# Performance work log

Hardware: AMD Instinct MI355X
Metric: run time of the kernel (lower is better)

## Reference

```python
import itertools
import jax, jax.numpy as jnp
import numpy as np

# ---- config (mirrors args) ----
BS = 8; C = 20              # 4 + num_sem_categories
FH, FW = 480, 640           # frame height/width
DU = 2                      # du_scale
NSC = 16                    # num_sem_categories
RES = 5; ZRES = 5           # xy / z map resolution (cm)
MAP_CM = 4800 // 2          # map_size_cm // global_downscaling
VR = 100                    # vision_range
HFOV = 79.0
MAXH = int(200 / ZRES); MINH = int(-40 / ZRES)   # 40, -8
AGENT_H = 0.88 * 100.0
CAT_T, EXP_T, MAP_T = 5.0, 1.0, 1.0
STAIR_R = 30
DEG = 57.29577951308232
M = MAP_CM // RES           # 480 local map cells

CAM_XC = (FW - 1.) / 2.
CAM_ZC = (FH - 1.) / 2.
CAM_F = (FW / 2.) / np.tan(np.deg2rad(HFOV / 2.))
SHIFT_X = VR * RES // 2     # shift_loc theta = pi/2 -> identity rotation, +x only

def _circle_mask(r):
    size = 2 * r
    ii, jj = np.meshgrid(np.arange(size), np.arange(size), indexing='ij')
    return (((ii + 0.5 - size // 2) ** 2 + (jj + 0.5 - size // 2) ** 2) <= r ** 2).astype(np.float32)

CIRCLE = jnp.asarray(_circle_mask(STAIR_R))

def splat_feat_nd(init_grid, feat, coords):
    # init_grid [B,F,d0,d1,d2], feat [B,F,N], coords [B,3,N] in [-1,1]
    B, nF = init_grid.shape[:2]
    gd = init_grid.shape[2:]
    grid_flat = init_grid.reshape(B, nF, -1)
    pos_dim, wts_dim = [], []
    for d in range(3):
        pos = coords[:, d, :] * gd[d] / 2 + gd[d] / 2
        pd, wd = [], []
        for ix in (0, 1):
            pos_ix = jnp.floor(pos) + ix
            safe = ((pos_ix > 0) & (pos_ix < gd[d])).astype(pos.dtype)
            wd.append((1 - jnp.abs(pos - pos_ix)) * safe)
            pd.append(pos_ix * safe)
        pos_dim.append(pd); wts_dim.append(wd)
    idxs, vals = [], []
    for ix_d in itertools.product((0, 1), repeat=3):  # 8 trilinear corners
        index = jnp.zeros_like(pos_dim[0][0])
        wts = jnp.ones_like(wts_dim[0][0])
        for d in range(3):
            index = index * gd[d] + pos_dim[d][ix_d[d]]
            wts = wts * wts_dim[d][ix_d[d]]
        idxs.append(index.astype(jnp.int32))
        vals.append(feat * wts[:, None, :])
    idx = jnp.concatenate(idxs, -1)          # [B, 8N]
    val = jnp.concatenate(vals, -1)          # [B, F, 8N]
    grid_flat = jax.vmap(lambda g, i, v: g.at[:, i].add(v))(grid_flat, idx, val)
    return jnp.round(grid_flat).reshape(init_grid.shape)

def affine_grid(theta, H, W):
    # F.affine_grid, align_corners=False (torch default)
    xs = (jnp.arange(W, dtype=theta.dtype) + 0.5) * 2 / W - 1
    ys = (jnp.arange(H, dtype=theta.dtype) + 0.5) * 2 / H - 1
    gy, gx = jnp.meshgrid(ys, xs, indexing='ij')
    base = jnp.stack([gx, gy, jnp.ones_like(gx)], -1)   # [H,W,3]
    return jnp.einsum('bij,hwj->bhwi', theta, base)     # [B,H,W,2]

def grid_sample(img, grid):
    # bilinear, zero padding, align_corners=True
    B, C_, H, W = img.shape
    gx = (grid[..., 0] + 1.) * (W - 1) / 2.
    gy = (grid[..., 1] + 1.) * (H - 1) / 2.
    x0 = jnp.floor(gx); y0 = jnp.floor(gy)
    def gather(ix, iy):
        valid = ((ix >= 0) & (ix < W) & (iy >= 0) & (iy < H)).astype(img.dtype)
        ic = jnp.clip(ix, 0, W - 1).astype(jnp.int32)
        jc = jnp.clip(iy, 0, H - 1).astype(jnp.int32)
        v = jax.vmap(lambda im, yy, xx: im[:, yy, xx])(img, jc, ic)  # [B,C,H,W]
        return v * valid[:, None]
    wx1 = gx - x0; wx0 = 1 - wx1; wy1 = gy - y0; wy0 = 1 - wy1
    return (gather(x0, y0) * (wx0 * wy0)[:, None]
            + gather(x0 + 1, y0) * (wx1 * wy0)[:, None]
            + gather(x0, y0 + 1) * (wx0 * wy1)[:, None]
            + gather(x0 + 1, y0 + 1) * (wx1 * wy1)[:, None])

def maxpool3(x):
    return jax.lax.reduce_window(x, -jnp.inf, jax.lax.max,
                                 (1, 1, 3, 3), (1, 1, 1, 1),
                                 [(0, 0), (0, 0), (1, 1), (1, 1)])

def _forward(obs, pose_obs, maps_last, poses_last, eve_angle):
    bs, c, h, w = obs.shape
    hs, ws = h // DU, w // DU
    depth = obs[:, 3, ::DU, ::DU]
    # point cloud from depth (du.get_point_cloud_from_z_t)
    xg = jnp.arange(0, w, DU, dtype=obs.dtype)[None, None, :]
    zg = (h - 1 - jnp.arange(0, h, DU, dtype=obs.dtype))[None, :, None]
    X = (xg - CAM_XC) * depth / CAM_F
    Z = (zg - CAM_ZC) * depth / CAM_F
    # camera elevation rotation about x-axis (per-env eve_angle) + sensor height
    th = jnp.deg2rad(eve_angle)[:, None, None]
    ct, st = jnp.cos(th), jnp.sin(th)
    Yr = ct * depth - st * Z
    Zr = st * depth + ct * Z + AGENT_H
    Xs = X + SHIFT_X
    # normalize to [-1,1] voxel coords
    cx = (Xs / RES - VR // 2) / VR * 2.0
    cy = (Yr / RES - VR // 2) / VR * 2.0
    cz = (Zr / ZRES - (MAXH + MINH) // 2) / (MAXH - MINH) * 2.0
    coords = jnp.stack([cx.reshape(bs, -1), cy.reshape(bs, -1), cz.reshape(bs, -1)], 1)
    sem = obs[:, 4:].reshape(bs, c - 4, hs, DU, ws, DU).mean((3, 5))  # AvgPool2d(du)
    feat = jnp.concatenate([jnp.ones((bs, 1, hs * ws), obs.dtype),
                            sem.reshape(bs, c - 4, hs * ws)], 1)
    init_grid = jnp.zeros((bs, 1 + NSC, VR, VR, MAXH - MINH), obs.dtype)
    voxels = splat_feat_nd(init_grid, feat, coords).transpose(0, 1, 3, 2, 4)
    min_z = int(25 / ZRES - MINH)
    max_z = int((AGENT_H + 50) / ZRES - MINH)
    mid_z = int(AGENT_H / ZRES - MINH)
    ah_proj = voxels[..., min_z:max_z].sum(-1)
    stair_proj = voxels[..., mid_z - 5:mid_z].sum(-1)
    all_proj = voxels.sum(-1)
    fp_map = jnp.clip(ah_proj[:, 0:1] / MAP_T, 0., 1.)
    fp_stair = jnp.clip(stair_proj[:, 0:1] / MAP_T, 0., 1.)
    fp_exp = jnp.clip(all_proj[:, 0:1] / EXP_T, 0., 1.)
    x1 = M // 2 - VR // 2; x2 = x1 + VR; y1 = M // 2; y2 = y1 + VR
    agent_view = jnp.zeros((bs, c, M, M), obs.dtype)
    agent_view = agent_view.at[:, 0:1, y1:y2, x1:x2].set(fp_map)
    agent_view = agent_view.at[:, 1:2, y1:y2, x1:x2].set(fp_exp)
    agent_view = agent_view.at[:, 4:, y1:y2, x1:x2].set(jnp.clip(ah_proj[:, 1:] / CAT_T, 0., 1.))
    agent_view_stair = jax.lax.stop_gradient(agent_view).at[:, 0:1, y1:y2, x1:x2].set(fp_stair)
    # pose integration (get_new_pose_batch)
    tr = poses_last[:, 2] / DEG
    ny = poses_last[:, 1] + pose_obs[:, 0] * jnp.sin(tr) + pose_obs[:, 1] * jnp.cos(tr)
    nx = poses_last[:, 0] + pose_obs[:, 0] * jnp.cos(tr) - pose_obs[:, 1] * jnp.sin(tr)
    no = poses_last[:, 2] + pose_obs[:, 2] * DEG
    no = jnp.fmod(no - 180.0, 360.0) + 180.0
    no = jnp.fmod(no + 180.0, 360.0) - 180.0
    current_poses = jnp.stack([nx, ny, no], 1)
    cp = jax.lax.stop_gradient(current_poses)  # st_pose = clone().detach()
    half = M // 2
    st_xy = -(cp[:, :2] * 100.0 / RES - half) / half
    st_t = (90.0 - cp[:, 2]) * np.pi / 180.0
    c_, s_ = jnp.cos(st_t), jnp.sin(st_t)
    zeros = jnp.zeros_like(c_); ones = jnp.ones_like(c_)
    theta1 = jnp.stack([jnp.stack([c_, -s_, zeros], 1), jnp.stack([s_, c_, zeros], 1)], 1)
    theta2 = jnp.stack([jnp.stack([ones, zeros, st_xy[:, 0]], 1),
                        jnp.stack([zeros, ones, st_xy[:, 1]], 1)], 1)
    rot_grid = affine_grid(theta1, M, M)
    trans_grid = affine_grid(theta2, M, M)
    translated = grid_sample(grid_sample(agent_view, rot_grid), trans_grid)
    diff = translated[:, 1:2] - maxpool3(translated[:, 0:1])
    diff = jnp.where(diff > 0.8, 1.0, 0.0).astype(obs.dtype)
    maps2 = jnp.maximum(maps_last, translated)
    m0 = (eve_angle == 0)[:, None, None, None] & (diff == 1.0)
    map_pred = maps2.at[:, 0:1].set(jnp.where(m0, 0.0, maps2[:, 0:1]))
    # stair map
    translated_stair = grid_sample(grid_sample(agent_view_stair, rot_grid), trans_grid)
    s_y = jnp.clip((cp[0, 1] * 100 / 5).astype(jnp.int32), STAIR_R, M - STAIR_R - 1)
    s_x = jnp.clip((cp[0, 0] * 100 / 5).astype(jnp.int32), STAIR_R, M - STAIR_R - 1)
    full_mask = jax.lax.dynamic_update_slice(jnp.zeros((M, M), obs.dtype), CIRCLE.astype(obs.dtype),
                                             (s_y - STAIR_R, s_x - STAIR_R))
    translated_stair = translated_stair.at[0, 0:2].multiply(full_mask)
    diff_s = translated_stair[:, 1:2] - translated_stair[:, 0:1]
    diff_s = jnp.where(diff_s > 0.8, 1.0, 0.0).astype(obs.dtype)
    maps3 = jnp.maximum(maps_last, translated_stair)
    m0s = (eve_angle == 0)[:, None, None, None] & (diff_s == 1.0)
    map_pred_stair = maps3.at[:, 0:1].set(jnp.where(m0s, 0.0, maps3[:, 0:1]))
    return translated, map_pred, map_pred_stair, current_poses

def setup_inputs() -> dict:
    key = jax.random.key(0)
    k1, k2, k3, k4, k5 = jax.random.split(key, 5)
    obs = jax.random.uniform(k1, (BS, C, FH, FW), jnp.float32)
    depth = 50.0 + 350.0 * jax.random.uniform(k2, (BS, FH, FW), jnp.float32)  # depth in cm
    obs = obs.at[:, 3].set(depth)
    pose_obs = jax.random.normal(k3, (BS, 3), jnp.float32) * jnp.array([0.1, 0.05, 0.02], jnp.float32)
    maps_last = jax.random.uniform(k4, (BS, C, M, M), jnp.float32)
    poses_last = (jnp.tile(jnp.array([12.0, 12.0, 0.0], jnp.float32), (BS, 1))
                  + jax.random.normal(k5, (BS, 3), jnp.float32) * jnp.array([0.5, 0.5, 30.0], jnp.float32))
    eve_angle = jnp.array([0., 0., -30., 0., 30., 0., 0., 0.], jnp.float32)
    return {'obs': obs, 'pose_obs': pose_obs, 'maps_last': maps_last,
            'poses_last': poses_last, 'eve_angle': eve_angle}

def reference(obs, pose_obs, maps_last, poses_last, eve_angle):
    return _forward(obs, pose_obs, maps_last, poses_last, eve_angle)
```

## Files before the change

kernel.cpp:

```cpp
#include <hip/hip_runtime.h>
#include <cmath>

#define NBS 8
#define NC 20
#define NFH 480
#define NFW 640
#define NHS 240
#define NWS 320
#define NM 480
#define NPIX (NM * NM)
#define NVR 100
#define NPIXELS (NBS * NHS * NWS)
#define PPB (NHS * NWS)
#define CPB 4

constexpr long long T_OFF    = 0LL;
constexpr long long P_OFF    = 36864000LL;
constexpr long long S_OFF    = 73728000LL;
constexpr long long POSE_OFF = 110592000LL;

constexpr long long SMAP_OFF = P_OFF;
constexpr long long PAR_OFF  = SMAP_OFF + 1520000LL;
constexpr long long REC_OFF  = PAR_OFF + 64LL;
constexpr long long EPOS_OFF = REC_OFF + 2457600LL;
constexpr long long ESEM_OFF = EPOS_OFF + 2457600LL;
constexpr long long CNT_OFF  = ESEM_OFF + 9830400LL;
constexpr long long OFF2_OFF = CNT_OFF + 80000LL;
constexpr long long CUR_OFF  = OFF2_OFF + 80000LL;

__device__ __forceinline__ float clamp01(float x) {
    return fminf(fmaxf(x, 0.0f), 1.0f);
}

__device__ __forceinline__ void project_px(const float* __restrict__ ob, float ev,
                                           float camf, int iy, int ix,
                                           float& posx, float& posy, float& posz,
                                           bool& alive, bool& semz) {
    float depth = ob[(3LL * NFH + 2 * iy) * NFW + 2 * ix];
    float th = ev * 0.017453292519943295f;
    float ct = cosf(th), st = sinf(th);
    float X = ((float)(2 * ix) - 319.5f) * depth / camf;
    float Z = ((float)(479 - 2 * iy) - 239.5f) * depth / camf;
    float Yr = ct * depth - st * Z;
    float Zr = st * depth + ct * Z + 88.0f;
    float Xs = X + 250.0f;
    float cx = ((Xs / 5.0f) - 50.0f) / 100.0f * 2.0f;
    float cy = ((Yr / 5.0f) - 50.0f) / 100.0f * 2.0f;
    float cz = ((Zr / 5.0f) - 16.0f) / 48.0f * 2.0f;
    posx = (cx * 100.0f) / 2.0f + 50.0f;
    posy = (cy * 100.0f) / 2.0f + 50.0f;
    posz = (cz * 48.0f) / 2.0f + 24.0f;
    alive = (posx > 0.0f) && (posx < 100.0f) &&
            (posy > 0.0f) && (posy < 100.0f) &&
            (posz > 0.0f) && (posz < 48.0f);
    semz = (posz > 12.0f) && (posz < 35.0f);
}

__global__ void k_pose(const float* __restrict__ pose_obs,
                       const float* __restrict__ poses_last,
                       float* __restrict__ outp) {
    int b = threadIdx.x;
    if (b >= NBS) return;
    float* pose_out = outp + POSE_OFF;
    float* par = outp + PAR_OFF;
    const float DEGf = 57.29577951308232f;
    float tr = poses_last[b * 3 + 2] / DEGf;
    float s_tr = sinf(tr), c_tr = cosf(tr);
    float ny = poses_last[b * 3 + 1] + pose_obs[b * 3 + 0] * s_tr + pose_obs[b * 3 + 1] * c_tr;
    float nx = poses_last[b * 3 + 0] + pose_obs[b * 3 + 0] * c_tr - pose_obs[b * 3 + 1] * s_tr;
    float no = poses_last[b * 3 + 2] + pose_obs[b * 3 + 2] * DEGf;
    no = fmodf(no - 180.0f, 360.0f) + 180.0f;
    no = fmodf(no + 180.0f, 360.0f) - 180.0f;
    pose_out[b * 3 + 0] = nx;
    pose_out[b * 3 + 1] = ny;
    pose_out[b * 3 + 2] = no;
    float stx = -((nx * 100.0f) / 5.0f - 240.0f) / 240.0f;
    float sty = -((ny * 100.0f) / 5.0f - 240.0f) / 240.0f;
    float stt = ((90.0f - no) * 3.14159265358979323846f) / 180.0f;
    par[b * 4 + 0] = cosf(stt);
    par[b * 4 + 1] = sinf(stt);
    par[b * 4 + 2] = stx;
    par[b * 4 + 3] = sty;
    if (b == 0) {
        int sy = (int)((ny * 100.0f) / 5.0f);
        int sx = (int)((nx * 100.0f) / 5.0f);
        sy = min(max(sy, 30), NM - 31);
        sx = min(max(sx, 30), NM - 31);
        par[32] = (float)sy;
        par[33] = (float)sx;
    }
}

__global__ void k_count(const float* __restrict__ obs,
                        const float* __restrict__ eve, float camf,
                        unsigned int* __restrict__ counts,
                        float4* __restrict__ rec) {
    int tid = blockIdx.x * blockDim.x + threadIdx.x;
    if (tid >= NPIXELS) return;
    int b = tid / PPB;
    int p = tid % PPB;
    int iy = p / NWS, ix = p % NWS;
    const float* ob = obs + (long long)b * NC * NFH * NFW;
    float posx, posy, posz;
    bool alive, semz;
    project_px(ob, eve[b], camf, iy, ix, posx, posy, posz, alive, semz);
    float flag = alive ? (semz ? 2.0f : 1.0f) : 0.0f;
    rec[tid] = make_float4(posx, posy, posz, flag);
    if (!alive) return;
    int fx = (int)floorf(posx);
    int fy = (int)floorf(posy);
    atomicAdd(&counts[b * 10000 + fx * 100 + fy], 1u);
}

__global__ void __launch_bounds__(1024) k_scan(const unsigned int* __restrict__ counts,
                                               unsigned int* __restrict__ offs,
                                               unsigned int* __restrict__ curs) {
    int b = blockIdx.x;
    int t = threadIdx.x;
    int lane = t & 63, wid = t >> 6;
    const unsigned int* cb = counts + b * 10000;
    unsigned int base_i = (unsigned int)t * 10u;
    unsigned int v[10];
    unsigned int s = 0;
#pragma unroll
    for (int k = 0; k < 10; ++k) {
        unsigned int i = base_i + (unsigned int)k;
        unsigned int x = (i < 10000u) ? cb[i] : 0u;
        v[k] = s;
        s += x;
    }
    unsigned int incl = s;
#pragma unroll
    for (int d = 1; d < 64; d <<= 1) {
        unsigned int u = __shfl_up(incl, d);
        if (lane >= d) incl += u;
    }
    __shared__ unsigned int wtot[16];
    __shared__ unsigned int wexc[16];
    if (lane == 63) wtot[wid] = incl;
    __syncthreads();
    if (t == 0) {
        unsigned int a = 0;
        for (int i = 0; i < 16; ++i) { wexc[i] = a; a += wtot[i]; }
    }
    __syncthreads();
    unsigned int tbase = wexc[wid] + (incl - s);
#pragma unroll
    for (int k = 0; k < 10; ++k) {
        unsigned int i = base_i + (unsigned int)k;
        if (i < 10000u) {
            unsigned int e = tbase + v[k];
            offs[b * 10000 + i] = e;
            curs[b * 10000 + i] = e;
        }
    }
}

__global__ void k_fill(const float* __restrict__ obs,
                       const float4* __restrict__ rec,
                       unsigned int* __restrict__ curs,
                       float4* __restrict__ epos,
                       float4* __restrict__ esem4) {
    int tid = blockIdx.x * blockDim.x + threadIdx.x;
    if (tid >= NPIXELS) return;
    float4 r = rec[tid];
    if (r.w == 0.0f) return;
    int b = tid / PPB;
    int p = tid % PPB;
    int iy = p / NWS, ix = p % NWS;
    int fx = (int)floorf(r.x);
    int fy = (int)floorf(r.y);
    unsigned int slot = atomicAdd(&curs[b * 10000 + fx * 100 + fy], 1u);
    long long gslot = (long long)b * PPB + slot;
    epos[gslot] = make_float4(r.x, r.y, r.z, 0.0f);
    if (r.w == 2.0f) {
        const float* ob = obs + (long long)b * NC * NFH * NFW;
        float sem[16];
#pragma unroll
        for (int k = 0; k < 16; ++k) {
            const float* q = ob + ((long long)(4 + k) * NFH + 2 * iy) * NFW + 2 * ix;
            sem[k] = (q[0] + q[1] + q[NFW] + q[NFW + 1]) * 0.25f;
        }
#pragma unroll
        for (int g = 0; g < 4; ++g)
            esem4[gslot * 4 + g] =
                make_float4(sem[4 * g], sem[4 * g + 1], sem[4 * g + 2], sem[4 * g + 3]);
    }
}

__global__ void __launch_bounds__(256) k_accum(const float4* __restrict__ epos,
                                               const float4* __restrict__ esem4,
                                               const unsigned int* __restrict__ counts,
                                               const unsigned int* __restrict__ offs,
                                               float* __restrict__ smap) {
    int wid = threadIdx.x >> 6, lane = threadIdx.x & 63;
    int col = blockIdx.x * CPB + wid;
    int b = col / 10000;
    int xy = col % 10000;
    int x = xy / 100, y = xy % 100;
    __shared__ float acc[CPB][400];
    float* A = acc[wid];
    for (int i = lane; i < 400; i += 64) A[i] = 0.0f;
    __syncthreads();
    if (x >= 1 && y >= 1) {
        int base = b * 10000;
        int b00 = base + (x - 1) * 100 + (y - 1);
        int b01 = base + (x - 1) * 100 + y;
        int b10 = base + x * 100 + (y - 1);
        int b11 = base + x * 100 + y;
        unsigned int s0 = offs[b00];
        unsigned int n0 = offs[b01] + counts[b01] - s0;
        unsigned int s1 = offs[b10];
        unsigned int n1 = offs[b11] + counts[b11] - s1;
        unsigned int E = n0 + n1;
        const float4* pb = epos + (long long)b * PPB;
        const float4* sb = esem4 + (long long)b * PPB * 4;
        float fx_ = (float)x, fy_ = (float)y;
        for (unsigned int t = lane; t < E; t += 64) {
            unsigned int idx = (t < n0) ? (s0 + t) : (s1 + (t - n0));
            float4 e = pb[idx];
            float wx = 1.0f - fabsf(e.x - fx_);
            float wy = 1.0f - fabsf(e.y - fy_);
            float wxy = wx * wy;
            if (wxy <= 0.0f) continue;
            float posz = e.z;
            float fz = floorf(posz);
            bool zsem = (posz > 12.0f) && (posz < 35.0f);
            float sem[16];
            if (zsem) {
#pragma unroll
                for (int g = 0; g < 4; ++g) {
                    float4 s4 = sb[(long long)idx * 4 + g];
                    sem[4 * g + 0] = s4.x; sem[4 * g + 1] = s4.y;
                    sem[4 * g + 2] = s4.z; sem[4 * g + 3] = s4.w;
                }
            }
#pragma unroll
            for (int d = 0; d < 2; ++d) {
                float zf = fz + (float)d;
                int z = (int)zf;
                if (z < 1 || z > 47) continue;
                float w = wxy * (1.0f - fabsf(posz - zf));
                if (w == 0.0f) continue;
                atomicAdd(&A[z], w);
                if (z >= 13 && z < 35) {
                    float* ap = A + 48 + (z - 13) * 16;
#pragma unroll
                    for (int k = 0; k < 16; ++k)
                        atomicAdd(ap + k, sem[k] * w);
                }
            }
        }
    }
    __syncthreads();
    float* smb = smap + (long long)b * 19 * 10000;
    int ij = y * 100 + x;
    if (lane < 16) {
        float s = 0.0f;
#pragma unroll
        for (int z = 13; z < 35; ++z) s += rintf(A[48 + (z - 13) * 16 + lane]);
        smb[(3 + lane) * 10000 + ij] = clamp01(s / 5.0f);
    } else if (lane == 16) {
        float s = 0.0f;
        for (int z = 13; z < 35; ++z) s += rintf(A[z]);
        smb[ij] = clamp01(s);
    } else if (lane == 17) {
        float s = 0.0f;
        for (int z = 0; z < 48; ++z) s += rintf(A[z]);
        smb[10000 + ij] = clamp01(s);
    } else if (lane == 18) {
        float s = 0.0f;
        for (int z = 20; z < 25; ++z) s += rintf(A[z]);
        smb[20000 + ij] = clamp01(s);
    }
}

__global__ void k_translate(float* __restrict__ outp,
                            const float* __restrict__ smap,
                            const float* __restrict__ par,
                            const float* __restrict__ maps_last,
                            const float* __restrict__ eve) {
    int tid = blockIdx.x * blockDim.x + threadIdx.x;
    if (tid >= NBS * NPIX) return;
    int b = tid / NPIX;
    int ij = tid % NPIX;
    int i = ij / NM, j = ij % NM;
    float c = par[b * 4 + 0], s = par[b * 4 + 1];
    float stx = par[b * 4 + 2], sty = par[b * 4 + 3];
    float gx = (((float)j + 0.5f) * 2.0f) / 480.0f - 1.0f;
    float gy = (((float)i + 0.5f) * 2.0f) / 480.0f - 1.0f;
    float px = ((gx + stx) + 1.0f) * 479.0f / 2.0f;
    float py = ((gy + sty) + 1.0f) * 479.0f / 2.0f;
    float x0 = floorf(px), y0 = floorf(py);
    float wx1 = px - x0, wx0 = 1.0f - wx1;
    float wy1 = py - y0, wy0 = 1.0f - wy1;
    int offs[16];
    float wts[16];
    int nt = 0;
#pragma unroll
    for (int t = 0; t < 4; ++t) {
        int ox = t & 1, oy = t >> 1;
        float xo = x0 + (float)ox, yo = y0 + (float)oy;
        if (!(xo >= 0.0f && xo < 480.0f && yo >= 0.0f && yo < 480.0f)) continue;
        float wo = (ox ? wx1 : wx0) * (oy ? wy1 : wy0);
        int ixo = (int)xo, iyo = (int)yo;
        float gx2 = (((float)ixo + 0.5f) * 2.0f) / 480.0f - 1.0f;
        float gy2 = (((float)iyo + 0.5f) * 2.0f) / 480.0f - 1.0f;
        float rx = c * gx2 - s * gy2;
        float ry = s * gx2 + c * gy2;
        float qx = (rx + 1.0f) * 479.0f / 2.0f;
        float qy = (ry + 1.0f) * 479.0f / 2.0f;
        float xq0 = floorf(qx), yq0 = floorf(qy);
        float u1 = qx - xq0, u0 = 1.0f - u1;
        float v1 = qy - yq0, v0 = 1.0f - v1;
#pragma unroll
        for (int t2 = 0; t2 < 4; ++t2) {
            int ax = t2 & 1, ay = t2 >> 1;
            float xa = xq0 + (float)ax, ya = yq0 + (float)ay;
            if (xa >= 190.0f && xa < 290.0f && ya >= 240.0f && ya < 340.0f) {
                float w = wo * ((ax ? u1 : u0) * (ay ? v1 : v0));
                if (w != 0.0f) {
                    offs[nt] = ((int)ya - 240) * 100 + ((int)xa - 190);
                    wts[nt] = w;
                    ++nt;
                }
            }
        }
    }
    float a0 = 0.0f, a1 = 0.0f, as_ = 0.0f;
    float cat[16];
#pragma unroll
    for (int k = 0; k < 16; ++k) cat[k] = 0.0f;
    if (nt > 0) {
        const float* sm = smap + (long long)b * 19 * 10000;
        for (int t = 0; t < nt; ++t) {
            float w = wts[t];
            int o = offs[t];
            a0 += w * sm[o];
            a1 += w * sm[10000 + o];
            as_ += w * sm[20000 + o];
#pragma unroll
            for (int k = 0; k < 16; ++k) cat[k] += w * sm[(3 + k) * 10000 + o];
        }
    }
    float* To = outp + T_OFF;
    long long obase = (long long)b * NC * NPIX + ij;
    To[obase] = a0;
    To[obase + (long long)NPIX] = a1;
    To[obase + 2LL * NPIX] = 0.0f;
    To[obase + 3LL * NPIX] = 0.0f;
#pragma unroll
    for (int k = 0; k < 16; ++k) To[obase + (long long)(4 + k) * NPIX] = cat[k];
    float ts0 = as_, t1s = a1;
    if (b == 0) {
        float dy = (float)i - par[32] + 0.5f;
        float dx = (float)j - par[33] + 0.5f;
        float mask = (dy * dy + dx * dx <= 900.0f) ? 1.0f : 0.0f;
        ts0 *= mask;
        t1s *= mask;
    }
    bool eve0 = (eve[b] == 0.0f);
    bool flag = (t1s - ts0) > 0.8f;
    const float* ml = maps_last + (long long)b * NC * NPIX;
    float* So = outp + S_OFF;
#pragma unroll
    for (int ch = 0; ch < NC; ++ch) {
        float tch = (ch == 0) ? ts0 : (ch == 1) ? t1s
                  : (ch < 4) ? 0.0f : cat[ch - 4];
        float m3 = fmaxf(ml[(long long)ch * NPIX + ij], tch);
        So[obase + (long long)ch * NPIX] = (ch == 0 && eve0 && flag) ? 0.0f : m3;
    }
}

__global__ void k_pred(const float* __restrict__ T, const float* __restrict__ maps_last,
                       const float* __restrict__ eve, float* __restrict__ outP) {
    int tid = blockIdx.x * blockDim.x + threadIdx.x;
    if (tid >= NBS * NPIX) return;
    int b = tid / NPIX;
    int ij = tid % NPIX;
    int i = ij / NM, j = ij % NM;
    const float* Tb = T + (long long)b * NC * NPIX;
    float mp = -INFINITY;
#pragma unroll
    for (int di = -1; di <= 1; ++di) {
        int ii = i + di;
        if (ii < 0 || ii >= NM) continue;
#pragma unroll
        for (int dj = -1; dj <= 1; ++dj) {
            int jj = j + dj;
            if (jj < 0 || jj >= NM) continue;
            mp = fmaxf(mp, Tb[(long long)ii * NM + jj]);
        }
    }
    float t1 = Tb[(long long)NPIX + ij];
    bool flag = (t1 - mp) > 0.8f;
    bool eve0 = (eve[b] == 0.0f);
    const float* ml = maps_last + (long long)b * NC * NPIX;
    long long obase = (long long)b * NC * NPIX + ij;
#pragma unroll
    for (int ch = 0; ch < NC; ++ch) {
        float m2 = fmaxf(ml[(long long)ch * NPIX + ij], Tb[(long long)ch * NPIX + ij]);
        outP[obase + (long long)ch * NPIX] = (ch == 0 && eve0 && flag) ? 0.0f : m2;
    }
}

extern "C" void kernel_launch(void* const* d_in, const int* in_sizes, int n_in,
                              void* d_out, int out_size, void* d_ws, size_t ws_size,
                              hipStream_t stream) {
    const float* obs = (const float*)d_in[0];
    const float* pose_obs = (const float*)d_in[1];
    const float* maps_last = (const float*)d_in[2];
    const float* poses_last = (const float*)d_in[3];
    const float* eve = (const float*)d_in[4];
    float* outp = (float*)d_out;

    float camf = (float)(320.0 / tan(39.5 * M_PI / 180.0));

    unsigned int* counts = (unsigned int*)(outp + CNT_OFF);
    unsigned int* offs2  = (unsigned int*)(outp + OFF2_OFF);
    unsigned int* curs   = (unsigned int*)(outp + CUR_OFF);
    float4* rec   = (float4*)(outp + REC_OFF);
    float4* epos  = (float4*)(outp + EPOS_OFF);
    float4* esem4 = (float4*)(outp + ESEM_OFF);

    hipMemsetAsync(counts, 0, 80000 * sizeof(unsigned int), stream);

    k_pose<<<1, 64, 0, stream>>>(pose_obs, poses_last, outp);

    k_count<<<NPIXELS / 256, 256, 0, stream>>>(obs, eve, camf, counts, rec);

    k_scan<<<NBS, 1024, 0, stream>>>(counts, offs2, curs);

    k_fill<<<NPIXELS / 256, 256, 0, stream>>>(obs, rec, curs, epos, esem4);

    k_accum<<<(NBS * 10000) / CPB, 256, 0, stream>>>(epos, esem4, counts, offs2,
                                                     outp + SMAP_OFF);

    k_translate<<<(NBS * NPIX) / 256, 256, 0, stream>>>(outp, outp + SMAP_OFF,
                                                        outp + PAR_OFF, maps_last, eve);

    k_pred<<<(NBS * NPIX) / 256, 256, 0, stream>>>(outp + T_OFF, maps_last, eve,
                                                   outp + P_OFF);
}
```

Baseline: 1.203 ms.

## Fuse pred into translate, restructure accum by y-strips, interleave splat map layout

```diff
diff --git a/kernel.cpp b/kernel.cpp
--- a/kernel.cpp
+++ b/kernel.cpp
@@ -9,24 +9,24 @@
 #define NWS 320
 #define NM 480
 #define NPIX (NM * NM)
-#define NVR 100
 #define NPIXELS (NBS * NHS * NWS)
 #define PPB (NHS * NWS)
-#define CPB 4
+#define YW 20
 
 constexpr long long T_OFF    = 0LL;
 constexpr long long P_OFF    = 36864000LL;
 constexpr long long S_OFF    = 73728000LL;
 constexpr long long POSE_OFF = 110592000LL;
 
-constexpr long long SMAP_OFF = P_OFF;
-constexpr long long PAR_OFF  = SMAP_OFF + 1520000LL;
-constexpr long long REC_OFF  = PAR_OFF + 64LL;
-constexpr long long EPOS_OFF = REC_OFF + 2457600LL;
-constexpr long long ESEM_OFF = EPOS_OFF + 2457600LL;
-constexpr long long CNT_OFF  = ESEM_OFF + 9830400LL;
-constexpr long long OFF2_OFF = CNT_OFF + 80000LL;
-constexpr long long CUR_OFF  = OFF2_OFF + 80000LL;
+constexpr long long SMAP_O = 0LL;
+constexpr long long PAR_O  = SMAP_O + 1600000LL;
+constexpr long long REC_O  = PAR_O + 64LL;
+constexpr long long EPOS_O = REC_O + 2457600LL;
+constexpr long long ESEM_O = EPOS_O + 2457600LL;
+constexpr long long CNT_O  = ESEM_O + 9830400LL;
+constexpr long long OFF_O  = CNT_O + 80000LL;
+constexpr long long CUR_O  = OFF_O + 80000LL;
+constexpr long long SCR_END = CUR_O + 80000LL;
 
 __device__ __forceinline__ float clamp01(float x) {
     return fminf(fmaxf(x, 0.0f), 1.0f);
@@ -58,11 +58,10 @@
 
 __global__ void k_pose(const float* __restrict__ pose_obs,
                        const float* __restrict__ poses_last,
-                       float* __restrict__ outp) {
+                       float* __restrict__ pose_out,
+                       float* __restrict__ par) {
     int b = threadIdx.x;
     if (b >= NBS) return;
-    float* pose_out = outp + POSE_OFF;
-    float* par = outp + PAR_OFF;
     const float DEGf = 57.29577951308232f;
     float tr = poses_last[b * 3 + 2] / DEGf;
     float s_tr = sinf(tr), c_tr = cosf(tr);
@@ -193,37 +192,38 @@
                                                const unsigned int* __restrict__ counts,
                                                const unsigned int* __restrict__ offs,
                                                float* __restrict__ smap) {
-    int wid = threadIdx.x >> 6, lane = threadIdx.x & 63;
-    int col = blockIdx.x * CPB + wid;
-    int b = col / 10000;
-    int xy = col % 10000;
-    int x = xy / 100, y = xy % 100;
-    __shared__ float acc[CPB][400];
-    float* A = acc[wid];
-    for (int i = lane; i < 400; i += 64) A[i] = 0.0f;
+    int blk = blockIdx.x;
+    int b = blk / 500;
+    int r = blk % 500;
+    int x = r / 5;
+    int y0 = (r % 5) * YW;
+    __shared__ float acc[YW][400];
+    int tid = threadIdx.x;
+    for (int i2 = tid; i2 < YW * 400; i2 += 256) (&acc[0][0])[i2] = 0.0f;
     __syncthreads();
-    if (x >= 1 && y >= 1) {
+    if (x >= 1) {
+        int byLo = max(y0 - 1, 0);
+        int byHi = min(y0 + YW - 1, 99);
         int base = b * 10000;
-        int b00 = base + (x - 1) * 100 + (y - 1);
-        int b01 = base + (x - 1) * 100 + y;
-        int b10 = base + x * 100 + (y - 1);
-        int b11 = base + x * 100 + y;
-        unsigned int s0 = offs[b00];
-        unsigned int n0 = offs[b01] + counts[b01] - s0;
-        unsigned int s1 = offs[b10];
-        unsigned int n1 = offs[b11] + counts[b11] - s1;
+        int s0i = base + (x - 1) * 100 + byLo;
+        int e0i = base + (x - 1) * 100 + byHi;
+        int s1i = base + x * 100 + byLo;
+        int e1i = base + x * 100 + byHi;
+        unsigned int st0 = offs[s0i];
+        unsigned int n0 = offs[e0i] + counts[e0i] - st0;
+        unsigned int st1 = offs[s1i];
+        unsigned int n1 = offs[e1i] + counts[e1i] - st1;
         unsigned int E = n0 + n1;
         const float4* pb = epos + (long long)b * PPB;
         const float4* sb = esem4 + (long long)b * PPB * 4;
-        float fx_ = (float)x, fy_ = (float)y;
-        for (unsigned int t = lane; t < E; t += 64) {
-            unsigned int idx = (t < n0) ? (s0 + t) : (s1 + (t - n0));
+        float xf = (float)x;
+        for (unsigned int t = tid; t < E; t += 256) {
+            unsigned int idx = (t < n0) ? (st0 + t) : (st1 + (t - n0));
             float4 e = pb[idx];
-            float wx = 1.0f - fabsf(e.x - fx_);
-            float wy = 1.0f - fabsf(e.y - fy_);
-            float wxy = wx * wy;
-            if (wxy <= 0.0f) continue;
-            float posz = e.z;
+            float wx = 1.0f - fabsf(e.x - xf);
+            if (wx <= 0.0f) continue;
+            float posy = e.y, posz = e.z;
+            int fyi = (int)floorf(posy);
             float fz = floorf(posz);
             bool zsem = (posz > 12.0f) && (posz < 35.0f);
             float sem[16];
@@ -236,57 +236,60 @@
                 }
             }
 #pragma unroll
-            for (int d = 0; d < 2; ++d) {
-                float zf = fz + (float)d;
-                int z = (int)zf;
-                if (z < 1 || z > 47) continue;
-                float w = wxy * (1.0f - fabsf(posz - zf));
-                if (w == 0.0f) continue;
-                atomicAdd(&A[z], w);
-                if (z >= 13 && z < 35) {
-                    float* ap = A + 48 + (z - 13) * 16;
-#pragma unroll
-                    for (int k = 0; k < 16; ++k)
-                        atomicAdd(ap + k, sem[k] * w);
+            for (int dy2 = 0; dy2 < 2; ++dy2) {
+                int cy = fyi + dy2;
+                if (cy < 1 || cy >= 100 || cy < y0 || cy >= y0 + YW) continue;
+                float w2 = wx * (1.0f - fabsf(posy - (float)cy));
+                if (w2 <= 0.0f) continue;
+                float* A = acc[cy - y0];
+#pragma unroll
+                for (int d = 0; d < 2; ++d) {
+                    float zf = fz + (float)d;
+                    int z = (int)zf;
+                    if (z < 1 || z > 47) continue;
+                    float w = w2 * (1.0f - fabsf(posz - zf));
+                    if (w == 0.0f) continue;
+                    atomicAdd(&A[z], w);
+                    if (z >= 13 && z < 35) {
+                        float* ap = A + 48 + (z - 13) * 16;
+#pragma unroll
+                        for (int k = 0; k < 16; ++k)
+                            atomicAdd(ap + k, sem[k] * w);
+                    }
                 }
             }
         }
     }
     __syncthreads();
-    float* smb = smap + (long long)b * 19 * 10000;
-    int ij = y * 100 + x;
-    if (lane < 16) {
+    float* smb = smap + (long long)b * 200000;
+    for (int o = tid; o < YW * 20; o += 256) {
+        int ly = o / 20, ch = o % 20;
+        int cy = y0 + ly;
+        const float* A = acc[ly];
         float s = 0.0f;
-#pragma unroll
-        for (int z = 13; z < 35; ++z) s += rintf(A[48 + (z - 13) * 16 + lane]);
-        smb[(3 + lane) * 10000 + ij] = clamp01(s / 5.0f);
-    } else if (lane == 16) {
-        float s = 0.0f;
-        for (int z = 13; z < 35; ++z) s += rintf(A[z]);
-        smb[ij] = clamp01(s);
-    } else if (lane == 17) {
-        float s = 0.0f;
-        for (int z = 0; z < 48; ++z) s += rintf(A[z]);
-        smb[10000 + ij] = clamp01(s);
-    } else if (lane == 18) {
-        float s = 0.0f;
-        for (int z = 20; z < 25; ++z) s += rintf(A[z]);
-        smb[20000 + ij] = clamp01(s);
-    }
-}
-
-__global__ void k_translate(float* __restrict__ outp,
-                            const float* __restrict__ smap,
-                            const float* __restrict__ par,
-                            const float* __restrict__ maps_last,
-                            const float* __restrict__ eve) {
-    int tid = blockIdx.x * blockDim.x + threadIdx.x;
-    if (tid >= NBS * NPIX) return;
-    int b = tid / NPIX;
-    int ij = tid % NPIX;
-    int i = ij / NM, j = ij % NM;
-    float c = par[b * 4 + 0], s = par[b * 4 + 1];
-    float stx = par[b * 4 + 2], sty = par[b * 4 + 3];
+        if (ch == 0) {
+            for (int z = 13; z < 35; ++z) s += rintf(A[z]);
+            s = clamp01(s);
+        } else if (ch == 1) {
+            for (int z = 0; z < 48; ++z) s += rintf(A[z]);
+            s = clamp01(s);
+        } else if (ch == 2) {
+            for (int z = 20; z < 25; ++z) s += rintf(A[z]);
+            s = clamp01(s);
+        } else if (ch < 19) {
+            int k = ch - 3;
+            for (int z = 13; z < 35; ++z) s += rintf(A[48 + (z - 13) * 16 + k]);
+            s = clamp01(s / 5.0f);
+        }
+        smb[(long long)(cy * 100 + x) * 20 + ch] = s;
+    }
+}
+
+template<bool FULL>
+__device__ __forceinline__ void eval_pix(int i, int j, const float* __restrict__ smb,
+                                         float c, float s, float stx, float sty,
+                                         float& a0, float& a1, float& as_, float* cat) {
+    a0 = 0.0f; a1 = 0.0f; as_ = 0.0f;
     float gx = (((float)j + 0.5f) * 2.0f) / 480.0f - 1.0f;
     float gy = (((float)i + 0.5f) * 2.0f) / 480.0f - 1.0f;
     float px = ((gx + stx) + 1.0f) * 479.0f / 2.0f;
@@ -294,9 +297,6 @@
     float x0 = floorf(px), y0 = floorf(py);
     float wx1 = px - x0, wx0 = 1.0f - wx1;
     float wy1 = py - y0, wy0 = 1.0f - wy1;
-    int offs[16];
-    float wts[16];
-    int nt = 0;
 #pragma unroll
     for (int t = 0; t < 4; ++t) {
         int ox = t & 1, oy = t >> 1;
@@ -320,37 +320,91 @@
             if (xa >= 190.0f && xa < 290.0f && ya >= 240.0f && ya < 340.0f) {
                 float w = wo * ((ax ? u1 : u0) * (ay ? v1 : v0));
                 if (w != 0.0f) {
-                    offs[nt] = ((int)ya - 240) * 100 + ((int)xa - 190);
-                    wts[nt] = w;
-                    ++nt;
+                    int o = ((int)ya - 240) * 100 + ((int)xa - 190);
+                    const float* bp = smb + (long long)o * 20;
+                    if constexpr (FULL) {
+                        const float4* b4 = (const float4*)bp;
+                        float4 v0_ = b4[0], v1_ = b4[1], v2_ = b4[2], v3_ = b4[3], v4_ = b4[4];
+                        a0 += w * v0_.x; a1 += w * v0_.y; as_ += w * v0_.z;
+                        cat[0]  += w * v0_.w;
+                        cat[1]  += w * v1_.x; cat[2]  += w * v1_.y;
+                        cat[3]  += w * v1_.z; cat[4]  += w * v1_.w;
+                        cat[5]  += w * v2_.x; cat[6]  += w * v2_.y;
+                        cat[7]  += w * v2_.z; cat[8]  += w * v2_.w;
+                        cat[9]  += w * v3_.x; cat[10] += w * v3_.y;
+                        cat[11] += w * v3_.z; cat[12] += w * v3_.w;
+                        cat[13] += w * v4_.x; cat[14] += w * v4_.y;
+                        cat[15] += w * v4_.z;
+                    } else {
+                        a0 += w * bp[0];
+                    }
                 }
             }
         }
     }
+}
+
+template<bool WRITEP>
+__global__ void __launch_bounds__(256) k_translate(float* __restrict__ outp,
+                                                   const float* __restrict__ smap,
+                                                   const float* __restrict__ par,
+                                                   const float* __restrict__ maps_last,
+                                                   const float* __restrict__ eve) {
+    int tid = blockIdx.x * blockDim.x + threadIdx.x;
+    int b = tid / NPIX;
+    int ij = tid % NPIX;
+    int i = ij / NM, j = ij % NM;
+    float c = par[b * 4 + 0], s = par[b * 4 + 1];
+    float stx = par[b * 4 + 2], sty = par[b * 4 + 3];
+    const float* smb = smap + (long long)b * 200000;
+    const float* ml = maps_last + (long long)b * NC * NPIX;
+    long long obase = (long long)b * NC * NPIX + ij;
+    bool eve0 = (eve[b] == 0.0f);
+
+    float gxp = (((float)j + 0.5f) * 2.0f) / 480.0f - 1.0f + stx;
+    float gyp = (((float)i + 0.5f) * 2.0f) / 480.0f - 1.0f + sty;
+    float rxp = c * gxp - s * gyp, ryp = s * gxp + c * gyp;
+    float qxc = (rxp + 1.0f) * 239.5f, qyc = (ryp + 1.0f) * 239.5f;
+    bool near_ = (qxc > 184.0f) && (qxc < 296.0f) && (qyc > 234.0f) && (qyc < 346.0f);
+
     float a0 = 0.0f, a1 = 0.0f, as_ = 0.0f;
     float cat[16];
 #pragma unroll
     for (int k = 0; k < 16; ++k) cat[k] = 0.0f;
-    if (nt > 0) {
-        const float* sm = smap + (long long)b * 19 * 10000;
-        for (int t = 0; t < nt; ++t) {
-            float w = wts[t];
-            int o = offs[t];
-            a0 += w * sm[o];
-            a1 += w * sm[10000 + o];
-            as_ += w * sm[20000 + o];
-#pragma unroll
-            for (int k = 0; k < 16; ++k) cat[k] += w * sm[(3 + k) * 10000 + o];
-        }
-    }
+    float mp = 0.0f;
+    if (near_) {
+        eval_pix<true>(i, j, smb, c, s, stx, sty, a0, a1, as_, cat);
+        if constexpr (WRITEP) {
+            mp = -INFINITY;
+#pragma unroll
+            for (int di = -1; di <= 1; ++di) {
+                int ii = i + di;
+                if (ii < 0 || ii >= NM) continue;
+#pragma unroll
+                for (int dj = -1; dj <= 1; ++dj) {
+                    int jj = j + dj;
+                    if (jj < 0 || jj >= NM) continue;
+                    float b0, b1, b2;
+                    if (di == 0 && dj == 0) b0 = a0;
+                    else eval_pix<false>(ii, jj, smb, c, s, stx, sty, b0, b1, b2, nullptr);
+                    mp = fmaxf(mp, b0);
+                }
+            }
+        }
+    }
+
+    float mlv[NC];
+#pragma unroll
+    for (int ch = 0; ch < NC; ++ch) mlv[ch] = ml[(long long)ch * NPIX + ij];
+
     float* To = outp + T_OFF;
-    long long obase = (long long)b * NC * NPIX + ij;
     To[obase] = a0;
     To[obase + (long long)NPIX] = a1;
     To[obase + 2LL * NPIX] = 0.0f;
     To[obase + 3LL * NPIX] = 0.0f;
 #pragma unroll
     for (int k = 0; k < 16; ++k) To[obase + (long long)(4 + k) * NPIX] = cat[k];
+
     float ts0 = as_, t1s = a1;
     if (b == 0) {
         float dy = (float)i - par[32] + 0.5f;
@@ -359,16 +413,26 @@
         ts0 *= mask;
         t1s *= mask;
     }
-    bool eve0 = (eve[b] == 0.0f);
-    bool flag = (t1s - ts0) > 0.8f;
-    const float* ml = maps_last + (long long)b * NC * NPIX;
+    bool flagS = (t1s - ts0) > 0.8f;
     float* So = outp + S_OFF;
 #pragma unroll
     for (int ch = 0; ch < NC; ++ch) {
         float tch = (ch == 0) ? ts0 : (ch == 1) ? t1s
                   : (ch < 4) ? 0.0f : cat[ch - 4];
-        float m3 = fmaxf(ml[(long long)ch * NPIX + ij], tch);
-        So[obase + (long long)ch * NPIX] = (ch == 0 && eve0 && flag) ? 0.0f : m3;
+        float m3 = fmaxf(mlv[ch], tch);
+        So[obase + (long long)ch * NPIX] = (ch == 0 && eve0 && flagS) ? 0.0f : m3;
+    }
+
+    if constexpr (WRITEP) {
+        bool flagP = (a1 - mp) > 0.8f;
+        float* Po = outp + P_OFF;
+#pragma unroll
+        for (int ch = 0; ch < NC; ++ch) {
+            float tch = (ch == 0) ? a0 : (ch == 1) ? a1
+                      : (ch < 4) ? 0.0f : cat[ch - 4];
+            float m2 = fmaxf(mlv[ch], tch);
+            Po[obase + (long long)ch * NPIX] = (ch == 0 && eve0 && flagP) ? 0.0f : m2;
+        }
     }
 }
 
@@ -416,16 +480,21 @@
 
     float camf = (float)(320.0 / tan(39.5 * M_PI / 180.0));
 
-    unsigned int* counts = (unsigned int*)(outp + CNT_OFF);
-    unsigned int* offs2  = (unsigned int*)(outp + OFF2_OFF);
-    unsigned int* curs   = (unsigned int*)(outp + CUR_OFF);
-    float4* rec   = (float4*)(outp + REC_OFF);
-    float4* epos  = (float4*)(outp + EPOS_OFF);
-    float4* esem4 = (float4*)(outp + ESEM_OFF);
+    bool useWS = (d_ws != nullptr) && (ws_size >= (size_t)SCR_END * 4);
+    float* scr = useWS ? (float*)d_ws : (outp + P_OFF);
+
+    float* smapp = scr + SMAP_O;
+    float* par   = scr + PAR_O;
+    float4* rec   = (float4*)(scr + REC_O);
+    float4* epos  = (float4*)(scr + EPOS_O);
+    float4* esem4 = (float4*)(scr + ESEM_O);
+    unsigned int* counts = (unsigned int*)(scr + CNT_O);
+    unsigned int* offs2  = (unsigned int*)(scr + OFF_O);
+    unsigned int* curs   = (unsigned int*)(scr + CUR_O);
 
     hipMemsetAsync(counts, 0, 80000 * sizeof(unsigned int), stream);
 
-    k_pose<<<1, 64, 0, stream>>>(pose_obs, poses_last, outp);
+    k_pose<<<1, 64, 0, stream>>>(pose_obs, poses_last, outp + POSE_OFF, par);
 
     k_count<<<NPIXELS / 256, 256, 0, stream>>>(obs, eve, camf, counts, rec);
 
@@ -433,12 +502,15 @@
 
     k_fill<<<NPIXELS / 256, 256, 0, stream>>>(obs, rec, curs, epos, esem4);
 
-    k_accum<<<(NBS * 10000) / CPB, 256, 0, stream>>>(epos, esem4, counts, offs2,
-                                                     outp + SMAP_OFF);
-
-    k_translate<<<(NBS * NPIX) / 256, 256, 0, stream>>>(outp, outp + SMAP_OFF,
-                                                        outp + PAR_OFF, maps_last, eve);
-
-    k_pred<<<(NBS * NPIX) / 256, 256, 0, stream>>>(outp + T_OFF, maps_last, eve,
-                                                   outp + P_OFF);
-}
+    k_accum<<<NBS * 500, 256, 0, stream>>>(epos, esem4, counts, offs2, smapp);
+
+    if (useWS) {
+        k_translate<true><<<(NBS * NPIX) / 256, 256, 0, stream>>>(outp, smapp, par,
+                                                                  maps_last, eve);
+    } else {
+        k_translate<false><<<(NBS * NPIX) / 256, 256, 0, stream>>>(outp, smapp, par,
+                                                                   maps_last, eve);
+        k_pred<<<(NBS * NPIX) / 256, 256, 0, stream>>>(outp + T_OFF, maps_last, eve,
+                                                       outp + P_OFF);
+    }
+}
```

New measurement: 1.129 ms. 1.07x faster.
